# Optimization experiments

Hardware: AMD Instinct MI355X
Metric: run time of the kernel (lower is better)

## Reference

```python
import jax, jax.numpy as jnp
import numpy as np

N = 50000
C_IN = 64
C_OUT = 64
K = 16
EPS = 1e-5


def _bn(x, g, b, m, v):
    # eval-mode BatchNorm1d over last dim
    return (x - m) * jax.lax.rsqrt(v + EPS) * g + b


def setup_inputs() -> dict:
    key = jax.random.key(0)
    ks = jax.random.split(key, 24)
    def lin(i, fan_in, fan_out):
        s = 1.0 / np.sqrt(fan_in)
        W = jax.random.uniform(ks[i], (fan_in, fan_out), jnp.float32, -s, s)
        b = jax.random.uniform(ks[i + 1], (fan_out,), jnp.float32, -s, s)
        return W, b
    Wq, bq = lin(0, C_IN, C_OUT)
    Wk, bk = lin(2, C_IN, C_OUT)
    Wv, bv = lin(4, C_IN, C_OUT)
    Wp, b_p = lin(6, 3, C_OUT)
    Wg1, bg1 = lin(8, C_OUT, C_OUT)
    Wg2, bg2 = lin(10, C_OUT, C_OUT)
    Wo, bo = lin(12, C_OUT, C_OUT)
    def bn_params(i):
        g = jax.random.uniform(ks[i], (C_OUT,), jnp.float32, 0.5, 1.5)
        b = jax.random.normal(ks[i + 1], (C_OUT,), jnp.float32) * 0.1
        m = jax.random.normal(ks[i + 2], (C_OUT,), jnp.float32) * 0.1
        v = jax.random.uniform(ks[i + 3], (C_OUT,), jnp.float32, 0.5, 1.5)
        return g, b, m, v
    bnp_g, bnp_b, bnp_m, bnp_v = bn_params(14)
    bng_g, bng_b, bng_m, bng_v = bn_params(18)
    points = jax.random.normal(ks[22], (N, 3), jnp.float32)
    features = jax.random.normal(ks[23], (N, C_IN), jnp.float32)
    grouped_indices = jax.random.randint(jax.random.fold_in(key, 7), (N, K), 0, N, jnp.int64 if jax.config.jax_enable_x64 else jnp.int32)
    return dict(points=points, features=features, grouped_indices=grouped_indices,
                Wq=Wq, bq=bq, Wk=Wk, bk=bk, Wv=Wv, bv=bv, Wp=Wp, b_p=b_p,
                bnp_g=bnp_g, bnp_b=bnp_b, bnp_m=bnp_m, bnp_v=bnp_v,
                Wg1=Wg1, bg1=bg1, bng_g=bng_g, bng_b=bng_b, bng_m=bng_m, bng_v=bng_v,
                Wg2=Wg2, bg2=bg2, Wo=Wo, bo=bo)


def reference(points, features, grouped_indices,
              Wq, bq, Wk, bk, Wv, bv, Wp, b_p,
              bnp_g, bnp_b, bnp_m, bnp_v,
              Wg1, bg1, bng_g, bng_b, bng_m, bng_v,
              Wg2, bg2, Wo, bo):
    q = features @ Wq + bq                      # (N, C)
    k = features @ Wk + bk
    v = features @ Wv + bv
    gpts = points[grouped_indices]              # (N, K, 3) gather
    gk = k[grouped_indices]                     # (N, K, C)
    gv = v[grouped_indices]                     # (N, K, C)
    rel = gpts - points[:, None, :]             # (N, K, 3)
    p = jax.nn.relu(_bn(rel @ Wp + b_p, bnp_g, bnp_b, bnp_m, bnp_v))  # (N, K, C)
    a = q[:, None, :] - gk + p                  # (N, K, C)
    h = jax.nn.relu(_bn(a @ Wg1 + bg1, bng_g, bng_b, bng_m, bng_v)) @ Wg2 + bg2
    attn = jax.nn.softmax(h, axis=1)            # softmax over neighbor axis
    out = jnp.sum((gv + p) * attn, axis=1) @ Wo + bo  # (N, C)
    return out
```

## Files before the change

kernel.cpp:

```cpp
#include <hip/hip_runtime.h>
#include <hip/hip_bf16.h>

#define EPSV 1e-5f
#define TW 4
#define TPW 8
#define SPD 76

typedef __attribute__((ext_vector_type(8))) short s8v;
typedef __attribute__((ext_vector_type(4))) float f4v;

struct InP {
  const float *points, *features; const int* gidx;
  const float *Wq,*bq,*Wk,*bk,*Wv,*bv,*Wp,*b_p;
  const float *bnp_g,*bnp_b,*bnp_m,*bnp_v;
  const float *Wg1,*bg1,*bng_g,*bng_b,*bng_m,*bng_v;
  const float *Wg2,*bg2,*Wo,*bo;
  float* out; int N;
};
struct WS {
  unsigned short *qW1;
  unsigned short *kvT;
  unsigned short *WAf, *Wkf, *Wvf, *W1f, *W2f, *Wof;
  unsigned short *Wpf;
  float *bq1F, *bpF, *bk1F;
};

__device__ __forceinline__ unsigned short f2bf(float x){
  __hip_bfloat16 h = __float2bfloat16(x);
  unsigned short u; __builtin_memcpy(&u, &h, 2); return u;
}
__device__ __forceinline__ float bf2f(unsigned short s){
  union{unsigned u; float f;} c; c.u = ((unsigned)s) << 16; return c.f;
}
__device__ __forceinline__ unsigned pk2(float x, float y){
  __hip_bfloat162 h = __float22bfloat162_rn(make_float2(x, y));
  unsigned u; __builtin_memcpy(&u, &h, 4); return u;
}
__device__ __forceinline__ s8v pack8(f4v x0, f4v x1){
  s8v r;
  ((unsigned*)&r)[0] = pk2(x0[0], x0[1]);
  ((unsigned*)&r)[1] = pk2(x0[2], x0[3]);
  ((unsigned*)&r)[2] = pk2(x1[0], x1[1]);
  ((unsigned*)&r)[3] = pk2(x1[2], x1[3]);
  return r;
}

__global__ void __launch_bounds__(256) prep_kernel(InP P, WS W){
  const int g = blockIdx.x*256 + threadIdx.x;
  const int e = g >> 3, j = g & 7;
  const int f = e >> 6, L = e & 63;
  const int ks = f & 1, nt = f >> 1;
  const int n = nt*16 + (L & 15);
  const int k = ks*32 + ((L >> 4) << 3) + j;
  const float sg = P.bng_g[n] * rsqrtf(P.bng_v[n] + EPSV);
  W.W1f[e*8+j] = f2bf(P.Wg1[k*64+n] * sg);
  W.W2f[e*8+j] = f2bf(P.Wg2[k*64+n]);
  W.Wof[e*8+j] = f2bf(P.Wo [k*64+n]);
  W.Wvf[e*8+j] = f2bf(P.Wv [k*64+n]);
  float acc = 0.f, acck = 0.f;
  #pragma unroll 8
  for (int d = 0; d < 64; d++){
    float w1 = P.Wg1[d*64+n];
    acc  += P.Wq[k*64+d] * w1;
    acck += P.Wk[k*64+d] * w1;
  }
  W.WAf[e*8+j] = f2bf(acc  * sg);
  W.Wkf[e*8+j] = f2bf(acck * sg);
  if (g < 2048){
    int ep = g >> 3;
    int ntp = ep >> 6, Lp = ep & 63;
    int np_ = ntp*16 + (Lp & 15);
    int kp = ((Lp >> 4) << 3) + j;
    float sp = P.bnp_g[np_] * rsqrtf(P.bnp_v[np_] + EPSV);
    W.Wpf[ep*8+j] = f2bf(kp < 3 ? P.Wp[kp*64+np_]*sp : 0.f);
  }
  if (g < 64){
    float sgt = P.bng_g[g] * rsqrtf(P.bng_v[g] + EPSV);
    float spt = P.bnp_g[g] * rsqrtf(P.bnp_v[g] + EPSV);
    float acc2 = 0.f, acck2 = 0.f;
    for (int d = 0; d < 64; d++){
      float w1 = P.Wg1[d*64+g];
      acc2  += P.bq[d] * w1;
      acck2 += P.bk[d] * w1;
    }
    W.bq1F[g] = acc2*sgt + P.bg1[g]*sgt + P.bng_b[g] - P.bng_m[g]*sgt;
    W.bk1F[g] = acck2*sgt;
    W.bpF[g]  = P.b_p[g]*spt + P.bnp_b[g] - P.bnp_m[g]*spt;
  }
}

__global__ void __launch_bounds__(256) qkv_kernel(InP P, WS W){
  const int tid = threadIdx.x;
  const int wid = tid >> 6, l = tid & 63;
  const int cl = l & 15, q = l >> 4;
  const int TILES = (P.N + 15) >> 4;
  const int task = blockIdx.x * TW + wid;
  if (task >= TILES) return;
  const int i0 = task * 16;
  int row = i0 + cl; if (row > P.N - 1) row = P.N - 1;
  const float* fr = P.features + (size_t)row*64 + q*8;
  f4v x0 = *(const f4v*)fr;
  f4v x1 = *(const f4v*)(fr + 4);
  s8v fa0 = pack8(x0, x1);
  x0 = *(const f4v*)(fr + 32);
  x1 = *(const f4v*)(fr + 36);
  s8v fa1 = pack8(x0, x1);

  auto doMat = [&](const unsigned short* Bf_, const float* biasPtr,
                   unsigned short* outPtr, int stride){
    const s8v* Bf = (const s8v*)Bf_;
    #pragma unroll
    for (int nt = 0; nt < 4; nt++){
      float bn = biasPtr[nt*16 + cl];
      f4v ci = { bn, bn, bn, bn };
      f4v c = __builtin_amdgcn_mfma_f32_16x16x32_bf16(fa0, Bf[(2*nt+0)*64 + l], ci, 0, 0, 0);
      c = __builtin_amdgcn_mfma_f32_16x16x32_bf16(fa1, Bf[(2*nt+1)*64 + l], c, 0, 0, 0);
      #pragma unroll
      for (int r = 0; r < 4; r++){
        int rg = i0 + q*4 + r;
        if (rg < P.N) outPtr[(size_t)rg*stride + nt*16 + cl] = f2bf(c[r]);
      }
    }
  };
  doMat(W.WAf, W.bq1F, W.qW1,      64);
  doMat(W.Wkf, W.bk1F, W.kvT,     128);
  doMat(W.Wvf, P.bv,   W.kvT + 64,128);
}

__global__ void __launch_bounds__(256, 2) main_kernel(InP P, WS W){
  __shared__ __align__(16) unsigned short Sp[TW][2][16*SPD];
  __shared__ __align__(16) unsigned short PreB[TW][TPW*SPD];
  __shared__ __align__(16) int sI[TW][TPW*16];
  const int tid = threadIdx.x;
  const int wid = tid >> 6, l = tid & 63;
  const int cl = l & 15, q = l >> 4;
  const int TILES = (P.N + TPW - 1) / TPW;
  const int task = blockIdx.x * TW + wid;
  if (task >= TILES) return;
  const int i0 = task * TPW;
  unsigned short* PreBw = PreB[wid];
  int* sIw = sI[wid];

  {
    long base = (long)i0*16 + l*2;
    long maxb = (long)P.N*16 - 2;
    if (base > maxb) base = maxb;
    int2 gi = *(const int2*)(P.gidx + base);
    *(int2*)&sIw[l*2] = gi;
  }

  s8v w1f[8], w2f[8], wpf[4];
  {
    const s8v* W1p = (const s8v*)W.W1f;
    const s8v* W2p = (const s8v*)W.W2f;
    const s8v* Wpp = (const s8v*)W.Wpf;
    #pragma unroll
    for (int f = 0; f < 8; f++){ w1f[f] = W1p[f*64 + l]; w2f[f] = W2p[f*64 + l]; }
    #pragma unroll
    for (int f = 0; f < 4; f++) wpf[f] = Wpp[f*64 + l];
  }
  float bp4[4], b24[4];
  #pragma unroll
  for (int nt = 0; nt < 4; nt++){ bp4[nt] = W.bpF[nt*16 + cl]; b24[nt] = P.bg2[nt*16 + cl]; }

  float ngx=0.f, ngy=0.f, ngz=0.f;
  {
    int nidx = sIw[cl];
    if (l < 16){ const float* gp = P.points + (size_t)nidx*3; ngx=gp[0]; ngy=gp[1]; ngz=gp[2]; }
  }
  float ncx = P.points[(size_t)i0*3+0];
  float ncy = P.points[(size_t)i0*3+1];
  float ncz = P.points[(size_t)i0*3+2];
  float nq0, nq1, nq2, nq3;
  {
    const unsigned short* qr = W.qW1 + (size_t)i0*64;
    nq0 = bf2f(qr[cl]); nq1 = bf2f(qr[16+cl]); nq2 = bf2f(qr[32+cl]); nq3 = bf2f(qr[48+cl]);
  }

  #pragma unroll 2
  for (int pt = 0; pt < TPW; pt++){
    unsigned short* Spw = Sp[wid][pt & 1];
    float gx=ngx, gy=ngy, gz=ngz, cx=ncx, cy=ncy, cz=ncz;
    float qcn4[4] = { nq0, nq1, nq2, nq3 };
    const bool valid = (i0 + pt < P.N);

    unsigned short kw[16], vv[16];
    {
      int4 vidx = *(const int4*)&sIw[pt*16 + q*4];
      #pragma unroll
      for (int r = 0; r < 4; r++){
        const unsigned short* vb = W.kvT + (size_t)vidx[r]*128 + cl;
        #pragma unroll
        for (int nt = 0; nt < 4; nt++){
          kw[nt*4+r] = vb[nt*16];
          vv[nt*4+r] = vb[64 + nt*16];
        }
      }
    }

    s8v ap;
    ((unsigned*)&ap)[0] = pk2(gx-cx, gy-cy);
    ((unsigned*)&ap)[1] = pk2(gz-cz, 0.f);
    ((unsigned*)&ap)[2] = 0u; ((unsigned*)&ap)[3] = 0u;
    f4v pc[4];
    #pragma unroll
    for (int nt = 0; nt < 4; nt++){
      f4v ci = { bp4[nt], bp4[nt], bp4[nt], bp4[nt] };
      pc[nt] = __builtin_amdgcn_mfma_f32_16x16x32_bf16(ap, wpf[nt], ci, 0, 0, 0);
    }
    #pragma unroll
    for (int nt = 0; nt < 4; nt++){
      #pragma unroll
      for (int r = 0; r < 4; r++){
        pc[nt][r] = fmaxf(pc[nt][r], 0.f);
        Spw[(q*4+r)*SPD + nt*16 + cl] = f2bf(pc[nt][r]);
      }
    }

    {
      int np = (pt + 1) & (TPW-1);
      int nidx = sIw[np*16 + cl];
      if (l < 16){ const float* gp = P.points + (size_t)nidx*3; ngx=gp[0]; ngy=gp[1]; ngz=gp[2]; }
      int ii = i0 + np; if (ii > P.N - 1) ii = P.N - 1;
      ncx = P.points[(size_t)ii*3+0];
      ncy = P.points[(size_t)ii*3+1];
      ncz = P.points[(size_t)ii*3+2];
      const unsigned short* qr = W.qW1 + (size_t)ii*64;
      nq0 = bf2f(qr[cl]); nq1 = bf2f(qr[16+cl]); nq2 = bf2f(qr[32+cl]); nq3 = bf2f(qr[48+cl]);
    }

    s8v af0 = *(const s8v*)&Spw[cl*SPD + q*8];
    s8v af1 = *(const s8v*)&Spw[cl*SPD + 32 + q*8];

    f4v tc[4];
    #pragma unroll
    for (int nt = 0; nt < 4; nt++){
      f4v ci = { qcn4[nt] - bf2f(kw[nt*4+0]),
                 qcn4[nt] - bf2f(kw[nt*4+1]),
                 qcn4[nt] - bf2f(kw[nt*4+2]),
                 qcn4[nt] - bf2f(kw[nt*4+3]) };
      tc[nt] = __builtin_amdgcn_mfma_f32_16x16x32_bf16(af0, w1f[2*nt+0], ci, 0, 0, 0);
      tc[nt] = __builtin_amdgcn_mfma_f32_16x16x32_bf16(af1, w1f[2*nt+1], tc[nt], 0, 0, 0);
      #pragma unroll
      for (int r = 0; r < 4; r++) tc[nt][r] = fmaxf(tc[nt][r], 0.f);
    }

    #pragma unroll
    for (int nt = 0; nt < 4; nt++)
      #pragma unroll
      for (int r = 0; r < 4; r++)
        Spw[(q*4+r)*SPD + nt*16 + cl] = f2bf(tc[nt][r]);
    s8v tf0 = *(const s8v*)&Spw[cl*SPD + q*8];
    s8v tf1 = *(const s8v*)&Spw[cl*SPD + 32 + q*8];

    f4v hc[4];
    #pragma unroll
    for (int nt = 0; nt < 4; nt++){
      f4v ci = { b24[nt], b24[nt], b24[nt], b24[nt] };
      hc[nt] = __builtin_amdgcn_mfma_f32_16x16x32_bf16(tf0, w2f[2*nt+0], ci, 0, 0, 0);
      hc[nt] = __builtin_amdgcn_mfma_f32_16x16x32_bf16(tf1, w2f[2*nt+1], hc[nt], 0, 0, 0);
    }

    float pre4[4];
    #pragma unroll
    for (int nt = 0; nt < 4; nt++){
      float s = 0.f, acc = 0.f;
      #pragma unroll
      for (int r = 0; r < 4; r++){
        float e2 = __expf(hc[nt][r]);
        s += e2;
        acc = fmaf(e2, bf2f(vv[nt*4+r]) + pc[nt][r], acc);
      }
      s += __shfl_xor(s, 16, 64);
      s += __shfl_xor(s, 32, 64);
      acc += __shfl_xor(acc, 16, 64);
      acc += __shfl_xor(acc, 32, 64);
      pre4[nt] = acc * __builtin_amdgcn_rcpf(s);
    }
    if (valid){
      float sa = (l & 16) ? pre4[1] : pre4[0];
      float sb = (l & 16) ? pre4[3] : pre4[2];
      PreBw[pt*SPD + l] = f2bf((l & 32) ? sb : sa);
    }
  }

  s8v wof[8];
  {
    const s8v* Wop = (const s8v*)W.Wof;
    #pragma unroll
    for (int f = 0; f < 8; f++) wof[f] = Wop[f*64 + l];
  }
  s8v ef0 = *(const s8v*)&PreBw[(cl & (TPW-1))*SPD + q*8];
  s8v ef1 = *(const s8v*)&PreBw[(cl & (TPW-1))*SPD + 32 + q*8];
  #pragma unroll
  for (int nt = 0; nt < 4; nt++){
    float bn = P.bo[nt*16 + cl];
    f4v ci = { bn, bn, bn, bn };
    f4v oc = __builtin_amdgcn_mfma_f32_16x16x32_bf16(ef0, wof[2*nt+0], ci, 0, 0, 0);
    oc = __builtin_amdgcn_mfma_f32_16x16x32_bf16(ef1, wof[2*nt+1], oc, 0, 0, 0);
    #pragma unroll
    for (int r = 0; r < 4; r++){
      int ro = q*4 + r;
      int rg = i0 + ro;
      if (ro < TPW && rg < P.N) P.out[(size_t)rg*64 + nt*16 + cl] = oc[r];
    }
  }
}

extern "C" void kernel_launch(void* const* d_in, const int* in_sizes, int n_in,
                              void* d_out, int out_size, void* d_ws, size_t ws_size,
                              hipStream_t stream){
  InP P;
  P.points   = (const float*)d_in[0];
  P.features = (const float*)d_in[1];
  P.gidx     = (const int*)d_in[2];
  P.Wq  = (const float*)d_in[3];  P.bq  = (const float*)d_in[4];
  P.Wk  = (const float*)d_in[5];  P.bk  = (const float*)d_in[6];
  P.Wv  = (const float*)d_in[7];  P.bv  = (const float*)d_in[8];
  P.Wp  = (const float*)d_in[9];  P.b_p = (const float*)d_in[10];
  P.bnp_g = (const float*)d_in[11]; P.bnp_b = (const float*)d_in[12];
  P.bnp_m = (const float*)d_in[13]; P.bnp_v = (const float*)d_in[14];
  P.Wg1 = (const float*)d_in[15]; P.bg1 = (const float*)d_in[16];
  P.bng_g = (const float*)d_in[17]; P.bng_b = (const float*)d_in[18];
  P.bng_m = (const float*)d_in[19]; P.bng_v = (const float*)d_in[20];
  P.Wg2 = (const float*)d_in[21]; P.bg2 = (const float*)d_in[22];
  P.Wo  = (const float*)d_in[23]; P.bo  = (const float*)d_in[24];
  P.out = (float*)d_out;
  const int N = in_sizes[0] / 3;
  P.N = N;

  WS W;
  char* w = (char*)d_ws;
  W.qW1 = (unsigned short*)w; w += (size_t)N*64*2;
  W.kvT = (unsigned short*)w; w += (size_t)N*128*2;
  W.WAf = (unsigned short*)w; w += 8*64*8*2;
  W.Wkf = (unsigned short*)w; w += 8*64*8*2;
  W.Wvf = (unsigned short*)w; w += 8*64*8*2;
  W.W1f = (unsigned short*)w; w += 8*64*8*2;
  W.W2f = (unsigned short*)w; w += 8*64*8*2;
  W.Wof = (unsigned short*)w; w += 8*64*8*2;
  W.Wpf = (unsigned short*)w; w += 4*64*8*2;
  W.bq1F = (float*)w; w += 256;
  W.bpF  = (float*)w; w += 256;
  W.bk1F = (float*)w; w += 256;

  const int TILES16 = (N + 15) / 16;
  const int grid16 = (TILES16 + TW - 1) / TW;
  const int TILESM = (N + TPW - 1) / TPW;
  const int gridM = (TILESM + TW - 1) / TW;
  hipLaunchKernelGGL(prep_kernel, dim3(16),     dim3(256), 0, stream, P, W);
  hipLaunchKernelGGL(qkv_kernel,  dim3(grid16), dim3(256), 0, stream, P, W);
  hipLaunchKernelGGL(main_kernel, dim3(gridM),  dim3(256), 0, stream, P, W);
}
```

Measured before the change: 204.1 us.

## Interleave k/v in bf16 pairs, prefetch next point's gather, compress registers

The qkv kernel now writes k and v interleaved per channel, so one 32-bit load fetches both values. The main kernel prefetches the next point's k/v gather one iteration ahead, keeping it in a register array that is copied at the start of each iteration. To offset that register cost, Wp fragments are reloaded from global memory each iteration, and the p activations are held as packed bf16. This aims to halve gather instructions and hide gather latency, but it adds extra loads per iteration and rounds p to bf16 in the value sum.

```diff
diff --git a/kernel.cpp b/kernel.cpp
--- a/kernel.cpp
+++ b/kernel.cpp
@@ -31,6 +31,12 @@
 }
 __device__ __forceinline__ float bf2f(unsigned short s){
   union{unsigned u; float f;} c; c.u = ((unsigned)s) << 16; return c.f;
+}
+__device__ __forceinline__ float bfLO(unsigned kv){
+  union{unsigned u; float f;} c; c.u = kv << 16; return c.f;
+}
+__device__ __forceinline__ float bfHI(unsigned kv){
+  union{unsigned u; float f;} c; c.u = kv & 0xffff0000u; return c.f;
 }
 __device__ __forceinline__ unsigned pk2(float x, float y){
   __hip_bfloat162 h = __float22bfloat162_rn(make_float2(x, y));
@@ -107,7 +113,7 @@
   s8v fa1 = pack8(x0, x1);
 
   auto doMat = [&](const unsigned short* Bf_, const float* biasPtr,
-                   unsigned short* outPtr, int stride){
+                   unsigned short* outPtr, int stride, int colMul, int colOff){
     const s8v* Bf = (const s8v*)Bf_;
     #pragma unroll
     for (int nt = 0; nt < 4; nt++){
@@ -118,13 +124,13 @@
       #pragma unroll
       for (int r = 0; r < 4; r++){
         int rg = i0 + q*4 + r;
-        if (rg < P.N) outPtr[(size_t)rg*stride + nt*16 + cl] = f2bf(c[r]);
+        if (rg < P.N) outPtr[(size_t)rg*stride + (nt*16+cl)*colMul + colOff] = f2bf(c[r]);
       }
     }
   };
-  doMat(W.WAf, W.bq1F, W.qW1,      64);
-  doMat(W.Wkf, W.bk1F, W.kvT,     128);
-  doMat(W.Wvf, P.bv,   W.kvT + 64,128);
+  doMat(W.WAf, W.bq1F, W.qW1,  64, 1, 0);
+  doMat(W.Wkf, W.bk1F, W.kvT, 128, 2, 0);
+  doMat(W.Wvf, P.bv,   W.kvT, 128, 2, 1);
 }
 
 __global__ void __launch_bounds__(256, 2) main_kernel(InP P, WS W){
@@ -149,20 +155,27 @@
     *(int2*)&sIw[l*2] = gi;
   }
 
-  s8v w1f[8], w2f[8], wpf[4];
+  s8v w1f[8], w2f[8];
   {
     const s8v* W1p = (const s8v*)W.W1f;
     const s8v* W2p = (const s8v*)W.W2f;
-    const s8v* Wpp = (const s8v*)W.Wpf;
     #pragma unroll
     for (int f = 0; f < 8; f++){ w1f[f] = W1p[f*64 + l]; w2f[f] = W2p[f*64 + l]; }
-    #pragma unroll
-    for (int f = 0; f < 4; f++) wpf[f] = Wpp[f*64 + l];
   }
   float bp4[4], b24[4];
   #pragma unroll
   for (int nt = 0; nt < 4; nt++){ bp4[nt] = W.bpF[nt*16 + cl]; b24[nt] = P.bg2[nt*16 + cl]; }
 
+  unsigned kwvv[16];
+  {
+    int4 vidx = *(const int4*)&sIw[q*4];
+    #pragma unroll
+    for (int r = 0; r < 4; r++){
+      const unsigned* vb = (const unsigned*)(W.kvT + (size_t)vidx[r]*128) + cl;
+      #pragma unroll
+      for (int nt = 0; nt < 4; nt++) kwvv[nt*4+r] = vb[nt*16];
+    }
+  }
   float ngx=0.f, ngy=0.f, ngz=0.f;
   {
     int nidx = sIw[cl];
@@ -180,21 +193,21 @@
   #pragma unroll 2
   for (int pt = 0; pt < TPW; pt++){
     unsigned short* Spw = Sp[wid][pt & 1];
+    unsigned kvc[16];
+    #pragma unroll
+    for (int i = 0; i < 16; i++) kvc[i] = kwvv[i];
     float gx=ngx, gy=ngy, gz=ngz, cx=ncx, cy=ncy, cz=ncz;
     float qcn4[4] = { nq0, nq1, nq2, nq3 };
     const bool valid = (i0 + pt < P.N);
 
-    unsigned short kw[16], vv[16];
     {
-      int4 vidx = *(const int4*)&sIw[pt*16 + q*4];
+      int np = (pt + 1) & (TPW-1);
+      int4 vidx = *(const int4*)&sIw[np*16 + q*4];
       #pragma unroll
       for (int r = 0; r < 4; r++){
-        const unsigned short* vb = W.kvT + (size_t)vidx[r]*128 + cl;
+        const unsigned* vb = (const unsigned*)(W.kvT + (size_t)vidx[r]*128) + cl;
         #pragma unroll
-        for (int nt = 0; nt < 4; nt++){
-          kw[nt*4+r] = vb[nt*16];
-          vv[nt*4+r] = vb[64 + nt*16];
-        }
+        for (int nt = 0; nt < 4; nt++) kwvv[nt*4+r] = vb[nt*16];
       }
     }
 
@@ -202,18 +215,24 @@
     ((unsigned*)&ap)[0] = pk2(gx-cx, gy-cy);
     ((unsigned*)&ap)[1] = pk2(gz-cz, 0.f);
     ((unsigned*)&ap)[2] = 0u; ((unsigned*)&ap)[3] = 0u;
-    f4v pc[4];
-    #pragma unroll
-    for (int nt = 0; nt < 4; nt++){
-      f4v ci = { bp4[nt], bp4[nt], bp4[nt], bp4[nt] };
-      pc[nt] = __builtin_amdgcn_mfma_f32_16x16x32_bf16(ap, wpf[nt], ci, 0, 0, 0);
-    }
-    #pragma unroll
-    for (int nt = 0; nt < 4; nt++){
-      #pragma unroll
-      for (int r = 0; r < 4; r++){
-        pc[nt][r] = fmaxf(pc[nt][r], 0.f);
-        Spw[(q*4+r)*SPD + nt*16 + cl] = f2bf(pc[nt][r]);
+    unsigned pcp[8];
+    {
+      const s8v* Wpp = (const s8v*)W.Wpf;
+      f4v pc[4];
+      #pragma unroll
+      for (int nt = 0; nt < 4; nt++){
+        f4v ci = { bp4[nt], bp4[nt], bp4[nt], bp4[nt] };
+        pc[nt] = __builtin_amdgcn_mfma_f32_16x16x32_bf16(ap, Wpp[nt*64 + l], ci, 0, 0, 0);
+      }
+      #pragma unroll
+      for (int nt = 0; nt < 4; nt++){
+        #pragma unroll
+        for (int r = 0; r < 4; r++){
+          pc[nt][r] = fmaxf(pc[nt][r], 0.f);
+          Spw[(q*4+r)*SPD + nt*16 + cl] = f2bf(pc[nt][r]);
+        }
+        pcp[nt*2+0] = pk2(pc[nt][0], pc[nt][1]);
+        pcp[nt*2+1] = pk2(pc[nt][2], pc[nt][3]);
       }
     }
 
@@ -235,10 +254,10 @@
     f4v tc[4];
     #pragma unroll
     for (int nt = 0; nt < 4; nt++){
-      f4v ci = { qcn4[nt] - bf2f(kw[nt*4+0]),
-                 qcn4[nt] - bf2f(kw[nt*4+1]),
-                 qcn4[nt] - bf2f(kw[nt*4+2]),
-                 qcn4[nt] - bf2f(kw[nt*4+3]) };
+      f4v ci = { qcn4[nt] - bfLO(kvc[nt*4+0]),
+                 qcn4[nt] - bfLO(kvc[nt*4+1]),
+                 qcn4[nt] - bfLO(kvc[nt*4+2]),
+                 qcn4[nt] - bfLO(kvc[nt*4+3]) };
       tc[nt] = __builtin_amdgcn_mfma_f32_16x16x32_bf16(af0, w1f[2*nt+0], ci, 0, 0, 0);
       tc[nt] = __builtin_amdgcn_mfma_f32_16x16x32_bf16(af1, w1f[2*nt+1], tc[nt], 0, 0, 0);
       #pragma unroll
@@ -264,12 +283,17 @@
     float pre4[4];
     #pragma unroll
     for (int nt = 0; nt < 4; nt++){
+      float p01lo = bf2f((unsigned short)(pcp[nt*2+0] & 0xffff));
+      float p01hi = bf2f((unsigned short)(pcp[nt*2+0] >> 16));
+      float p23lo = bf2f((unsigned short)(pcp[nt*2+1] & 0xffff));
+      float p23hi = bf2f((unsigned short)(pcp[nt*2+1] >> 16));
+      float pv[4] = { p01lo, p01hi, p23lo, p23hi };
       float s = 0.f, acc = 0.f;
       #pragma unroll
       for (int r = 0; r < 4; r++){
         float e2 = __expf(hc[nt][r]);
         s += e2;
-        acc = fmaf(e2, bf2f(vv[nt*4+r]) + pc[nt][r], acc);
+        acc = fmaf(e2, bfHI(kvc[nt*4+r]) + pv[r], acc);
       }
       s += __shfl_xor(s, 16, 64);
       s += __shfl_xor(s, 32, 64);
```

After: 204.4 us. No clear change (+0.1%).
